# Kernel tuning notes

Hardware: AMD Instinct MI355X
Metric: run time of the kernel (lower is better)

Reference implementation:

```python
import jax, jax.numpy as jnp
import numpy as np

N_TOKENS = 3
EMBED = 10
RNN = 10
N_LABELS = 3
B = 16384
T = 99
EPS = 1e-7  # keras CategoricalCrossentropy clip epsilon


def setup_inputs() -> dict:
    key = jax.random.key(0)
    ks = jax.random.split(key, 8)
    token_ids = jax.random.randint(ks[0], (B, T), 0, N_TOKENS, dtype=jnp.int32)
    label_ids = jax.random.randint(ks[1], (B, T), 0, N_LABELS)
    labels = jax.nn.one_hot(label_ids, N_LABELS, dtype=jnp.float32)
    mask = jnp.ones((B, T), dtype=bool)  # accepted by call() but unused, kept for signature fidelity
    emb_table = jax.random.normal(ks[2], (N_TOKENS, EMBED), jnp.float32) * 0.05
    W = jax.random.normal(ks[3], (EMBED, RNN), jnp.float32) / np.sqrt(EMBED)
    U = jax.random.normal(ks[4], (RNN, RNN), jnp.float32) / np.sqrt(RNN)
    b = jnp.zeros((RNN,), jnp.float32)
    Wo = jax.random.normal(ks[5], (RNN, N_LABELS), jnp.float32) / np.sqrt(RNN)
    bo = jnp.zeros((N_LABELS,), jnp.float32)
    return dict(token_ids=token_ids, labels=labels, mask=mask,
                emb_table=emb_table, W=W, U=U, b=b, Wo=Wo, bo=bo)


def reference(token_ids, labels, mask, emb_table, W, U, b, Wo, bo):
    # Embedding lookup (mask_zero=True -> token 0 is a masked step)
    emb = emb_table[token_ids]                      # [B, T, E]
    step_mask = (token_ids != 0)                    # [B, T]

    def step(h, inp):
        x_t, m_t = inp                              # [B, E], [B]
        h_new = jnp.tanh(x_t @ W + h @ U + b)       # SimpleRNN cell
        # Keras masking: masked timesteps carry previous state/output
        h = jnp.where(m_t[:, None], h_new, h)
        return h, h

    h0 = jnp.zeros((token_ids.shape[0], W.shape[1]), emb.dtype)
    _, states_tb = jax.lax.scan(step, h0, (emb.transpose(1, 0, 2), step_mask.T))
    states = states_tb.transpose(1, 0, 2)           # [B, T, R]

    probs = jax.nn.softmax(states @ Wo + bo, axis=-1)   # Dense(softmax) -> [B, T, L]
    probs_c = jnp.clip(probs, EPS, 1.0)
    loss = jnp.mean(-jnp.sum(labels * jnp.log(probs_c), axis=-1))
    accuracy = jnp.mean((jnp.argmax(probs, axis=-1) == jnp.argmax(labels, axis=-1)).astype(jnp.float32))
    return states, probs, accuracy, loss
```

## Files before the change

kernel.cpp:

```cpp
#include <hip/hip_runtime.h>
#include <math.h>

#define BB 16384
#define TT 99
#define RR 10
#define LL 3
#define TILE 33

__device__ __forceinline__ float fast_tanh(float x) {
    float e = __expf(2.0f * x);
    return fmaf(-2.0f, __builtin_amdgcn_rcpf(e + 1.0f), 1.0f);
}

__global__ __launch_bounds__(256, 2)
void rnn_state_kernel(const int* __restrict__ tok_ids,
                      const float* __restrict__ emb,
                      const float* __restrict__ U,
                      const float* __restrict__ W,
                      const float* __restrict__ bvec,
                      float* __restrict__ states_out)
{
    __shared__ __align__(16) float         s_st[4][8 * TILE * RR];
    __shared__                unsigned char s_tk[4][8 * 100];

    const int tid = threadIdx.x;
    const int w   = tid >> 6;
    const int l   = tid & 63;
    const int r8  = l >> 3;
    const int g   = l & 7;
    const int rb  = l & 56;
    const int rowbase = blockIdx.x * 32 + w * 8;

#pragma unroll
    for (int i = 0; i < 13; ++i) {
        const int q = l + 64 * i;
        if (q < 8 * TT) {
            const int tk = tok_ids[(size_t)rowbase * TT + q];
            const int r  = q / TT;
            s_tk[w][q + r] = (unsigned char)tk;
        }
    }

    const int jg0 = g;
    const int jg1 = (g < 2) ? 8 + g : g;
    float U0[RR], U1[RR];
    float c10 = bvec[jg0], c20 = c10;
    float c11 = bvec[jg1], c21 = c11;
#pragma unroll
    for (int i = 0; i < RR; ++i) {
        U0[i] = U[i * RR + jg0];
        U1[i] = U[i * RR + jg1];
        const float w0 = W[i * RR + jg0];
        const float w1 = W[i * RR + jg1];
        c10 = fmaf(emb[RR + i],     w0, c10);
        c20 = fmaf(emb[2 * RR + i], w0, c20);
        c11 = fmaf(emb[RR + i],     w1, c11);
        c21 = fmaf(emb[2 * RR + i], w1, c21);
    }

    float ho0 = 0.0f, ho1 = 0.0f;
    int sel = (int)s_tk[w][r8 * 100 + 0];

#pragma unroll 1
    for (int k = 0; k < 3; ++k) {
#pragma unroll 1
        for (int tt = 0; tt < TILE; ++tt) {
            const int t   = k * TILE + tt;
            const int cur = sel;
            const int tn  = (t + 1 < TT) ? t + 1 : t;
            sel = (int)s_tk[w][r8 * 100 + tn];

            float h[RR];
#pragma unroll
            for (int i = 0; i < 8; ++i) h[i] = __shfl(ho0, rb + i, 64);
            h[8] = __shfl(ho1, rb + 0, 64);
            h[9] = __shfl(ho1, rb + 1, 64);

            float a0 = (cur == 1) ? c10 : c20;
            float a1 = (cur == 1) ? c11 : c21;
#pragma unroll
            for (int i = 0; i < RR; ++i) {
                a0 = fmaf(h[i], U0[i], a0);
                a1 = fmaf(h[i], U1[i], a1);
            }
            const float hn0 = fast_tanh(a0);
            const float hn1 = fast_tanh(a1);
            if (cur != 0) { ho0 = hn0; ho1 = hn1; }

            float* sp = &s_st[w][r8 * (TILE * RR) + tt * RR];
            sp[g] = ho0;
            if (g < 2) sp[8 + g] = ho1;
        }

        const size_t gb = (size_t)rowbase * (TT * RR) + (size_t)k * (TILE * RR);
#pragma unroll
        for (int i = 0; i < 21; ++i) {
            const int q = l + 64 * i;
            if (q < 1320) {
                const int r = q / 165;
                const int m = q - r * 165;
                const float2 v = *reinterpret_cast<const float2*>(
                    &s_st[w][r * (TILE * RR) + 2 * m]);
                *reinterpret_cast<float2*>(
                    &states_out[gb + (size_t)r * (TT * RR) + 2 * m]) = v;
            }
        }
    }
}

__global__ __launch_bounds__(256)
void epilogue_kernel(const float* __restrict__ states,
                     const float* __restrict__ labels,
                     const float* __restrict__ Wo,
                     const float* __restrict__ bo,
                     float* __restrict__ probs_out,
                     float* __restrict__ ws)
{
    const int NT     = BB * TT;
    const int tid    = blockIdx.x * 256 + threadIdx.x;
    const int stride = 2048 * 256;

    float Wc0[RR], Wc1[RR], Wc2[RR];
#pragma unroll
    for (int j = 0; j < RR; ++j) {
        Wc0[j] = Wo[j * LL + 0];
        Wc1[j] = Wo[j * LL + 1];
        Wc2[j] = Wo[j * LL + 2];
    }
    const float b0 = bo[0], b1 = bo[1], b2 = bo[2];

    float loss = 0.0f;
    int   corr = 0;

#pragma unroll 1
    for (int idx = tid; idx < NT; idx += stride) {
        const float* hp = states + (size_t)idx * RR;
        float h[RR];
#pragma unroll
        for (int j = 0; j < RR; j += 2) {
            const float2 v = *reinterpret_cast<const float2*>(hp + j);
            h[j] = v.x; h[j + 1] = v.y;
        }
        const float la1 = labels[(size_t)idx * LL + 1];
        const float la2 = labels[(size_t)idx * LL + 2];
        const int   y   = (la1 > 0.5f) ? 1 : ((la2 > 0.5f) ? 2 : 0);

        float l0 = b0, l1 = b1, l2 = b2;
#pragma unroll
        for (int j = 0; j < RR; ++j) {
            l0 = fmaf(h[j], Wc0[j], l0);
            l1 = fmaf(h[j], Wc1[j], l1);
            l2 = fmaf(h[j], Wc2[j], l2);
        }
        const float e0 = __expf(l0), e1 = __expf(l1), e2 = __expf(l2);
        const float S  = e0 + e1 + e2;
        const float rs = __builtin_amdgcn_rcpf(S);
        probs_out[(size_t)idx * LL + 0] = e0 * rs;
        probs_out[(size_t)idx * LL + 1] = e1 * rs;
        probs_out[(size_t)idx * LL + 2] = e2 * rs;

        const float ly = (y == 0) ? l0 : ((y == 1) ? l1 : l2);
        loss += fminf(__logf(S) - ly, 16.11809565f);

        int ap = 0; float pm = l0;
        if (l1 > pm) { ap = 1; pm = l1; }
        if (l2 > pm) { ap = 2; }
        corr += (ap == y) ? 1 : 0;
    }

    __shared__ float sl[4], sc[4];
    float ls = loss, cs = (float)corr;
#pragma unroll
    for (int off = 32; off > 0; off >>= 1) {
        ls += __shfl_down(ls, off, 64);
        cs += __shfl_down(cs, off, 64);
    }
    if ((threadIdx.x & 63) == 0) { sl[threadIdx.x >> 6] = ls; sc[threadIdx.x >> 6] = cs; }
    __syncthreads();
    if (threadIdx.x == 0) {
        ws[blockIdx.x]        = sl[0] + sl[1] + sl[2] + sl[3];
        ws[2048 + blockIdx.x] = sc[0] + sc[1] + sc[2] + sc[3];
    }
}

__global__ __launch_bounds__(256)
void finalize_kernel(const float* __restrict__ ws, float* __restrict__ out_tail)
{
    __shared__ float sl[4], sc[4];
    const int t = threadIdx.x;
    float ls = 0.0f, cs = 0.0f;
#pragma unroll
    for (int i = 0; i < 8; ++i) {
        ls += ws[t + 256 * i];
        cs += ws[2048 + t + 256 * i];
    }
#pragma unroll
    for (int off = 32; off > 0; off >>= 1) {
        ls += __shfl_down(ls, off, 64);
        cs += __shfl_down(cs, off, 64);
    }
    if ((t & 63) == 0) { sl[t >> 6] = ls; sc[t >> 6] = cs; }
    __syncthreads();
    if (t == 0) {
        const float L = sl[0] + sl[1] + sl[2] + sl[3];
        const float C = sc[0] + sc[1] + sc[2] + sc[3];
        const float inv = 1.0f / (float)((size_t)BB * TT);
        out_tail[0] = C * inv;
        out_tail[1] = L * inv;
    }
}

extern "C" void kernel_launch(void* const* d_in, const int* in_sizes, int n_in,
                              void* d_out, int out_size, void* d_ws, size_t ws_size,
                              hipStream_t stream)
{
    const int*   tok    = (const int*)  d_in[0];
    const float* labels = (const float*)d_in[1];
    const float* emb = (const float*)d_in[3];
    const float* W   = (const float*)d_in[4];
    const float* U   = (const float*)d_in[5];
    const float* bv  = (const float*)d_in[6];
    const float* Wo  = (const float*)d_in[7];
    const float* bo  = (const float*)d_in[8];

    float* out    = (float*)d_out;
    float* states = out;
    float* probs  = out + (size_t)BB * TT * RR;
    float* tail   = out + (size_t)BB * TT * (RR + LL);
    float* ws     = (float*)d_ws;

    rnn_state_kernel<<<BB / 32, 256, 0, stream>>>(tok, emb, U, W, bv, states);
    epilogue_kernel<<<2048, 256, 0, stream>>>(states, labels, Wo, bo, probs, ws);
    finalize_kernel<<<1, 256, 0, stream>>>(ws, tail);
}
```

Measured before the change: 57.79 us.

## Fuse softmax/loss/accuracy epilogue into the RNN recurrence kernel

Removes the separate epilogue kernel and computes the output projection, softmax probabilities, loss and accuracy per tile directly from the shared-memory state buffer after each 33-step tile. This avoids re-reading the full states tensor from global memory and one kernel launch. The cost is extra work and register pressure inside the latency-bound recurrent kernel, which runs only 512 blocks. The epilogue work is also serialized per wave between tiles instead of being spread across a wide grid. Per-wave partial sums are written straight to the workspace, 2048 entries, and the existing finalize kernel reduces them.

```diff
diff --git a/kernel.cpp b/kernel.cpp
--- a/kernel.cpp
+++ b/kernel.cpp
@@ -13,14 +13,19 @@
 }
 
 __global__ __launch_bounds__(256, 2)
-void rnn_state_kernel(const int* __restrict__ tok_ids,
+void rnn_fused_kernel(const int* __restrict__ tok_ids,
+                      const float* __restrict__ labels,
                       const float* __restrict__ emb,
+                      const float* __restrict__ W,
                       const float* __restrict__ U,
-                      const float* __restrict__ W,
                       const float* __restrict__ bvec,
-                      float* __restrict__ states_out)
+                      const float* __restrict__ Wo,
+                      const float* __restrict__ bo,
+                      float* __restrict__ states_out,
+                      float* __restrict__ probs_out,
+                      float* __restrict__ ws)
 {
-    __shared__ __align__(16) float         s_st[4][8 * TILE * RR];
+    __shared__ __align__(16) float          s_st[4][8 * TILE * RR];
     __shared__                unsigned char s_tk[4][8 * 100];
 
     const int tid = threadIdx.x;
@@ -59,6 +64,8 @@
     }
 
     float ho0 = 0.0f, ho1 = 0.0f;
+    float loss = 0.0f;
+    int   corr = 0;
     int sel = (int)s_tk[w][r8 * 100 + 0];
 
 #pragma unroll 1
@@ -92,7 +99,9 @@
             if (g < 2) sp[8 + g] = ho1;
         }
 
+        const int    t0 = k * TILE;
         const size_t gb = (size_t)rowbase * (TT * RR) + (size_t)k * (TILE * RR);
+
 #pragma unroll
         for (int i = 0; i < 21; ++i) {
             const int q = l + 64 * i;
@@ -105,81 +114,56 @@
                     &states_out[gb + (size_t)r * (TT * RR) + 2 * m]) = v;
             }
         }
-    }
-}
-
-__global__ __launch_bounds__(256)
-void epilogue_kernel(const float* __restrict__ states,
-                     const float* __restrict__ labels,
-                     const float* __restrict__ Wo,
-                     const float* __restrict__ bo,
-                     float* __restrict__ probs_out,
-                     float* __restrict__ ws)
-{
-    const int NT     = BB * TT;
-    const int tid    = blockIdx.x * 256 + threadIdx.x;
-    const int stride = 2048 * 256;
-
-    float Wc0[RR], Wc1[RR], Wc2[RR];
-#pragma unroll
-    for (int j = 0; j < RR; ++j) {
-        Wc0[j] = Wo[j * LL + 0];
-        Wc1[j] = Wo[j * LL + 1];
-        Wc2[j] = Wo[j * LL + 2];
-    }
-    const float b0 = bo[0], b1 = bo[1], b2 = bo[2];
-
-    float loss = 0.0f;
-    int   corr = 0;
-
-#pragma unroll 1
-    for (int idx = tid; idx < NT; idx += stride) {
-        const float* hp = states + (size_t)idx * RR;
-        float h[RR];
-#pragma unroll
-        for (int j = 0; j < RR; j += 2) {
-            const float2 v = *reinterpret_cast<const float2*>(hp + j);
-            h[j] = v.x; h[j + 1] = v.y;
-        }
-        const float la1 = labels[(size_t)idx * LL + 1];
-        const float la2 = labels[(size_t)idx * LL + 2];
-        const int   y   = (la1 > 0.5f) ? 1 : ((la2 > 0.5f) ? 2 : 0);
-
-        float l0 = b0, l1 = b1, l2 = b2;
-#pragma unroll
-        for (int j = 0; j < RR; ++j) {
-            l0 = fmaf(h[j], Wc0[j], l0);
-            l1 = fmaf(h[j], Wc1[j], l1);
-            l2 = fmaf(h[j], Wc2[j], l2);
-        }
-        const float e0 = __expf(l0), e1 = __expf(l1), e2 = __expf(l2);
-        const float S  = e0 + e1 + e2;
-        const float rs = __builtin_amdgcn_rcpf(S);
-        probs_out[(size_t)idx * LL + 0] = e0 * rs;
-        probs_out[(size_t)idx * LL + 1] = e1 * rs;
-        probs_out[(size_t)idx * LL + 2] = e2 * rs;
-
-        const float ly = (y == 0) ? l0 : ((y == 1) ? l1 : l2);
-        loss += fminf(__logf(S) - ly, 16.11809565f);
-
-        int ap = 0; float pm = l0;
-        if (l1 > pm) { ap = 1; pm = l1; }
-        if (l2 > pm) { ap = 2; }
-        corr += (ap == y) ? 1 : 0;
-    }
-
-    __shared__ float sl[4], sc[4];
+
+#pragma unroll
+        for (int i = 0; i < 5; ++i) {
+            const int p = l + 64 * i;
+            if (p < 8 * TILE) {
+                const int r  = p / TILE;
+                const int tt = p - r * TILE;
+                const size_t idx = (size_t)(rowbase + r) * TT + t0 + tt;
+
+                const float* hp = &s_st[w][r * (TILE * RR) + tt * RR];
+                float l0 = bo[0], l1 = bo[1], l2 = bo[2];
+#pragma unroll
+                for (int j = 0; j < RR; ++j) {
+                    const float hj = hp[j];
+                    l0 = fmaf(hj, Wo[j * LL + 0], l0);
+                    l1 = fmaf(hj, Wo[j * LL + 1], l1);
+                    l2 = fmaf(hj, Wo[j * LL + 2], l2);
+                }
+                const float e0 = __expf(l0), e1 = __expf(l1), e2 = __expf(l2);
+                const float S  = e0 + e1 + e2;
+                const float rs = __builtin_amdgcn_rcpf(S);
+                probs_out[idx * LL + 0] = e0 * rs;
+                probs_out[idx * LL + 1] = e1 * rs;
+                probs_out[idx * LL + 2] = e2 * rs;
+
+                const float la1 = labels[idx * LL + 1];
+                const float la2 = labels[idx * LL + 2];
+                const int   y   = (la1 > 0.5f) ? 1 : ((la2 > 0.5f) ? 2 : 0);
+
+                const float ly = (y == 0) ? l0 : ((y == 1) ? l1 : l2);
+                loss += fminf(__logf(S) - ly, 16.11809565f);
+
+                int ap = 0; float pm = l0;
+                if (l1 > pm) { ap = 1; pm = l1; }
+                if (l2 > pm) { ap = 2; }
+                corr += (ap == y) ? 1 : 0;
+            }
+        }
+    }
+
     float ls = loss, cs = (float)corr;
 #pragma unroll
     for (int off = 32; off > 0; off >>= 1) {
         ls += __shfl_down(ls, off, 64);
         cs += __shfl_down(cs, off, 64);
     }
-    if ((threadIdx.x & 63) == 0) { sl[threadIdx.x >> 6] = ls; sc[threadIdx.x >> 6] = cs; }
-    __syncthreads();
-    if (threadIdx.x == 0) {
-        ws[blockIdx.x]        = sl[0] + sl[1] + sl[2] + sl[3];
-        ws[2048 + blockIdx.x] = sc[0] + sc[1] + sc[2] + sc[3];
+    if (l == 0) {
+        const int wid = blockIdx.x * 4 + w;
+        ws[wid]        = ls;
+        ws[2048 + wid] = cs;
     }
 }
 
@@ -229,7 +213,7 @@
     float* tail   = out + (size_t)BB * TT * (RR + LL);
     float* ws     = (float*)d_ws;
 
-    rnn_state_kernel<<<BB / 32, 256, 0, stream>>>(tok, emb, U, W, bv, states);
-    epilogue_kernel<<<2048, 256, 0, stream>>>(states, labels, Wo, bo, probs, ws);
+    rnn_fused_kernel<<<BB / 32, 256, 0, stream>>>(tok, labels, emb, W, U, bv, Wo, bo,
+                                                  states, probs, ws);
     finalize_kernel<<<1, 256, 0, stream>>>(ws, tail);
 }
```

Measured after the change: 50.10 us. -13.3%, faster.
